# Kernel tuning notes

Hardware: AMD Instinct MI355X
Metric: run time of the kernel (lower is better)

## Reference

```python
import jax, jax.numpy as jnp
import numpy as np

RATIO = 0.8
V, F, E = 100000, 128, 3200000


def setup_inputs() -> dict:
    key = jax.random.key(0)
    k0, k1, k2, k3 = jax.random.split(key, 4)
    verts = jax.random.normal(k0, (V, F), jnp.float32)
    edges = jax.random.randint(k1, (E, 2), 0, V, dtype=jnp.int32)
    verts_idx = jnp.arange(V, dtype=jnp.int32)
    edges_idx = jnp.arange(E, dtype=jnp.int32)
    # GraphConv(in_channels=128, out=1): w0 applied to verts, w1 to summed neighbors
    w0_w = jax.random.normal(k2, (1, F), jnp.float32) * 0.05
    w0_b = jnp.zeros((1,), jnp.float32)
    w1_w = jax.random.normal(k3, (1, F), jnp.float32) * 0.05
    w1_b = jnp.zeros((1,), jnp.float32)
    return dict(verts=verts, edges=edges, verts_idx=verts_idx, edges_idx=edges_idx,
                w0_w=w0_w, w0_b=w0_b, w1_w=w1_w, w1_b=w1_b)


def graph_conv(verts, edges, w0_w, w0_b, w1_w, w1_b):
    # pytorch3d-style GraphConv: w0(v_i) + sum_{j in N(i)} w1(v_j), symmetric edges
    nv = verts.shape[0]
    vw0 = verts @ w0_w.T + w0_b            # [V,1]
    vw1 = verts @ w1_w.T + w1_b            # [V,1]
    row, col = edges[:, 0], edges[:, 1]
    nbr = jax.ops.segment_sum(vw1[col], row, num_segments=nv)
    nbr = nbr + jax.ops.segment_sum(vw1[row], col, num_segments=nv)
    return vw0 + nbr                       # [V,1]


def reference(verts, edges, verts_idx, edges_idx, w0_w, w0_b, w1_w, w1_b):
    nv = verts.shape[0]
    attn = graph_conv(verts, edges, w0_w, w0_b, w1_w, w1_b)[:, 0]  # [V]
    k = int(nv * RATIO)
    _, mask_idx = jax.lax.top_k(attn, k)
    mask_idx = jnp.sort(mask_idx)                                   # [K]
    # scatter new compacted ids into a -1 mask
    mask = jnp.full((nv,), -1, dtype=jnp.int32).at[mask_idx].set(
        jnp.arange(k, dtype=jnp.int32))
    row = mask[edges[:, 0]]
    col = mask[edges[:, 1]]
    valid = (row >= 0) & (col >= 0)
    # jit-safe compaction: stable-sort valid edges to the front, pad rest with -1
    order = jnp.argsort(~valid, stable=True)
    new_edges = jnp.stack([row, col], axis=1)[order]                # [E,2]
    valid_s = valid[order]
    new_edges = jnp.where(valid_s[:, None], new_edges, -1)
    n_edges = valid.sum()
    verts_up = verts[mask_idx] * jnp.tanh(attn[mask_idx])[:, None]  # [K,F]
    verts_idx_up = verts_idx[:k]
    edges_idx_up = jnp.where(valid_s, edges_idx[order], -1)
    return verts_up, new_edges, verts_idx_up, edges_idx_up, n_edges
```

## Files before the change

### kernel.cpp

```cpp
#include <hip/hip_runtime.h>
#include <math.h>

#define TPB 256
#define SCAN_ITEMS 4
#define SCAN_BLOCK (TPB * SCAN_ITEMS)
#define TIECAP 2048
#define HIST_BLOCKS 104
#define BW 512
#define BUCKET_BLOCKS 256
#define BIG 1024

static __device__ __forceinline__ int block_scan_excl(int v, int* lds, int& total)
{
    int lane = threadIdx.x & 63;
    int wid  = threadIdx.x >> 6;
    int x = v;
#pragma unroll
    for (int off = 1; off < 64; off <<= 1) {
        int y = __shfl_up(x, off, 64);
        if (lane >= off) x += y;
    }
    if (lane == 63) lds[wid] = x;
    __syncthreads();
    int t0 = lds[0], t1 = lds[1], t2 = lds[2], t3 = lds[3];
    int wOff = (wid > 0 ? t0 : 0) + (wid > 1 ? t1 : 0) + (wid > 2 ? t2 : 0);
    total = t0 + t1 + t2 + t3;
    __syncthreads();
    return wOff + x - v;
}

__global__ void k_init(unsigned* hist, unsigned* state, int k,
                       unsigned* cursor, int NB, int CAP)
{
    int i = threadIdx.x;
    for (int j = i; j < 1024; j += blockDim.x) hist[j] = 0u;
    if (cursor) {
        for (int j = i; j < NB; j += blockDim.x)
            cursor[j * 16] = (unsigned)(j * CAP);
    }
    if (i == 0) {
        state[0] = 0u;
        state[1] = (unsigned)k;
        state[2] = 0u;
        state[3] = 0u;
        state[4] = 0u;
    }
}

__global__ void k_dots(const float* __restrict__ verts,
                       const float* __restrict__ w0, const float* __restrict__ b0,
                       const float* __restrict__ w1, const float* __restrict__ b1,
                       long long* __restrict__ iacc, long long* __restrict__ s1q, int V)
{
    int gid  = blockIdx.x * blockDim.x + threadIdx.x;
    int v    = gid >> 6;
    int lane = gid & 63;
    if (v >= V) return;
    const float2 a  = ((const float2*)(verts + (size_t)v * 128))[lane];
    const float2 wa = ((const float2*)w0)[lane];
    const float2 wb = ((const float2*)w1)[lane];
    float p0 = a.x * wa.x + a.y * wa.y;
    float p1 = a.x * wb.x + a.y * wb.y;
#pragma unroll
    for (int off = 32; off > 0; off >>= 1) {
        p0 += __shfl_down(p0, off, 64);
        p1 += __shfl_down(p1, off, 64);
    }
    if (lane == 0) {
        double s0 = (double)p0 + (double)b0[0];
        double s1 = (double)p1 + (double)b1[0];
        iacc[v] = (long long)llrint(s0 * 1099511627776.0);
        s1q[v]  = (long long)llrint(s1 * 1099511627776.0);
    }
}

__global__ void k_scatter(const int2* __restrict__ edges, const long long* __restrict__ s1q,
                          unsigned long long* __restrict__ iacc, int E)
{
    int i = blockIdx.x * blockDim.x + threadIdx.x;
    if (i >= E) return;
    int2 e = edges[i];
    atomicAdd(&iacc[e.x], (unsigned long long)s1q[e.y]);
    atomicAdd(&iacc[e.y], (unsigned long long)s1q[e.x]);
}

__global__ void __launch_bounds__(BIG)
k_bucket(const int2* __restrict__ edges, unsigned* __restrict__ bdata,
         unsigned* __restrict__ cursor, int E, int NB, int CAP, int chunk)
{
    __shared__ unsigned cnt[256];
    __shared__ unsigned base[256];
    const int tid   = threadIdx.x;
    const int start = blockIdx.x * chunk;
    const int end   = min(E, start + chunk);
    for (int j = tid; j < 256; j += BIG) cnt[j] = 0u;
    __syncthreads();
    for (int i = start + tid; i < end; i += BIG) {
        int2 e = edges[i];
        atomicAdd(&cnt[e.x >> 9], 1u);
        atomicAdd(&cnt[e.y >> 9], 1u);
    }
    __syncthreads();
    if (tid < NB) {
        unsigned c = cnt[tid];
        base[tid] = c ? atomicAdd(&cursor[tid * 16], c) : 0u;
        cnt[tid] = 0u;
    }
    __syncthreads();
    for (int i = start + tid; i < end; i += BIG) {
        int2 e = edges[i];
        int b0 = e.x >> 9;
        unsigned p0 = base[b0] + atomicAdd(&cnt[b0], 1u);
        if (p0 < (unsigned)(b0 + 1) * (unsigned)CAP)
            bdata[p0] = ((unsigned)e.y << 9) | (unsigned)(e.x & 511);
        int b1 = e.y >> 9;
        unsigned p1 = base[b1] + atomicAdd(&cnt[b1], 1u);
        if (p1 < (unsigned)(b1 + 1) * (unsigned)CAP)
            bdata[p1] = ((unsigned)e.x << 9) | (unsigned)(e.y & 511);
    }
}

__global__ void __launch_bounds__(BIG)
k_bucket_sum(const unsigned* __restrict__ bdata, const unsigned* __restrict__ cursor,
             const long long* __restrict__ s1q, const long long* __restrict__ iacc,
             float* __restrict__ attnf, unsigned* __restrict__ keys,
             unsigned* __restrict__ hist, int V, int CAP)
{
    __shared__ unsigned long long acc[BW];
    __shared__ unsigned lh[256];
    const int b   = blockIdx.x;
    const int tid = threadIdx.x;
    for (int j = tid; j < BW;  j += BIG) acc[j] = 0ull;
    for (int j = tid; j < 256; j += BIG) lh[j] = 0u;
    __syncthreads();
    unsigned n = cursor[b * 16] - (unsigned)(b * CAP);
    if (n > (unsigned)CAP) n = (unsigned)CAP;
    const unsigned* src = bdata + (size_t)b * CAP;
    for (unsigned i = tid; i < n; i += BIG) {
        unsigned p = src[i];
        atomicAdd(&acc[p & 511u], (unsigned long long)s1q[p >> 9]);
    }
    __syncthreads();
    for (int j = tid; j < BW; j += BIG) {
        int v = b * BW + j;
        if (v < V) {
            long long tot = iacc[v] + (long long)acc[j];
            float a = (float)((double)tot * 9.094947017729282379150390625e-13);
            attnf[v] = a;
            unsigned u = __float_as_uint(a);
            unsigned key = (u & 0x80000000u) ? ~u : (u | 0x80000000u);
            keys[v] = key;
            atomicAdd(&lh[key >> 24], 1u);
        }
    }
    __syncthreads();
    for (int j = tid; j < 256; j += BIG) {
        unsigned c = lh[j];
        if (c) atomicAdd(&hist[j], c);
    }
}

__global__ void k_finalize(const long long* __restrict__ iacc, float* __restrict__ attnf,
                           unsigned* __restrict__ keys, int V)
{
    int i = blockIdx.x * blockDim.x + threadIdx.x;
    if (i >= V) return;
    float a = (float)((double)iacc[i] * 9.094947017729282379150390625e-13);
    attnf[i] = a;
    unsigned u = __float_as_uint(a);
    keys[i] = (u & 0x80000000u) ? ~u : (u | 0x80000000u);
}

__global__ void k_hist(const unsigned* __restrict__ keys, int V,
                       const unsigned* __restrict__ state, int shift,
                       unsigned* __restrict__ hist)
{
    __shared__ unsigned lh[256];
    lh[threadIdx.x] = 0u;
    __syncthreads();
    unsigned pref = 0u;
    if (shift != 24) pref = state[0] >> (shift + 8);
    int stride = gridDim.x * blockDim.x;
    for (int i = blockIdx.x * blockDim.x + threadIdx.x; i < V; i += stride) {
        unsigned key = keys[i];
        bool ok = (shift == 24) || ((key >> (shift + 8)) == pref);
        if (ok) atomicAdd(&lh[(key >> shift) & 255u], 1u);
    }
    __syncthreads();
    unsigned c = lh[threadIdx.x];
    if (c) atomicAdd(&hist[threadIdx.x], c);
}

__global__ void k_select(const unsigned* __restrict__ hist, int shift, unsigned* __restrict__ state)
{
    if (threadIdx.x != 0 || blockIdx.x != 0) return;
    unsigned kk = state[1];
    unsigned cum = 0;
    int j = 255;
    for (; j > 0; --j) {
        unsigned c = hist[j];
        if (cum + c >= kk) break;
        cum += c;
    }
    state[0] |= ((unsigned)j) << shift;
    state[1] = kk - cum;
    if (shift == 0) state[2] = state[0];
}

__global__ void k_mark(const unsigned* __restrict__ keys, int V,
                       unsigned* __restrict__ state, int* __restrict__ selFlag,
                       int* __restrict__ tieList, unsigned* __restrict__ bsums)
{
    __shared__ int lds[4];
    const unsigned T = state[2];
    int base = blockIdx.x * SCAN_BLOCK + threadIdx.x * SCAN_ITEMS;
    int f[4] = {0, 0, 0, 0};
    unsigned kv[4];
    bool full = (base + 3 < V);
    if (full) {
        uint4 q = *(const uint4*)(keys + base);
        kv[0] = q.x; kv[1] = q.y; kv[2] = q.z; kv[3] = q.w;
    } else {
#pragma unroll
        for (int t = 0; t < 4; ++t)
            kv[t] = (base + t < V) ? keys[base + t] : 0u;
    }
#pragma unroll
    for (int t = 0; t < 4; ++t) {
        if (base + t < V) {
            f[t] = kv[t] > T ? 1 : 0;
            if (kv[t] == T) {
                unsigned p = atomicAdd(&state[3], 1u);
                if (p < TIECAP) tieList[p] = base + t;
            }
        }
    }
    if (full) {
        *(int4*)(selFlag + base) = make_int4(f[0], f[1], f[2], f[3]);
    } else {
#pragma unroll
        for (int t = 0; t < 4; ++t)
            if (base + t < V) selFlag[base + t] = f[t];
    }
    int tot;
    block_scan_excl(f[0] + f[1] + f[2] + f[3], lds, tot);
    if (threadIdx.x == 0) bsums[blockIdx.x] = (unsigned)tot;
}

__global__ void k_tie_resolve(const unsigned* __restrict__ state,
                              const int* __restrict__ tieList, int* __restrict__ selFlag,
                              unsigned* __restrict__ bsums)
{
    __shared__ int s[TIECAP];
    int n  = (int)state[3];
    if (n > TIECAP) n = TIECAP;
    int kk = (int)state[1];
    int tid = threadIdx.x;
    if (kk >= n) {
        for (int i = tid; i < n; i += blockDim.x) {
            int v = tieList[i];
            selFlag[v] = 1;
            atomicAdd(&bsums[v / SCAN_BLOCK], 1u);
        }
        return;
    }
    for (int i = tid; i < n; i += blockDim.x) s[i] = tieList[i];
    __syncthreads();
    for (int i = tid; i < n; i += blockDim.x) {
        int v = s[i];
        int r = 0;
        for (int j = 0; j < n; ++j) r += (s[j] < v);
        if (r < kk) {
            selFlag[v] = 1;
            atomicAdd(&bsums[v / SCAN_BLOCK], 1u);
        }
    }
}

__global__ void k_scanB(unsigned* __restrict__ sums, int nb,
                        unsigned* __restrict__ totalOut, float* __restrict__ outF)
{
    __shared__ int lds[4];
    int tid = threadIdx.x;
    int running = 0;
    for (int base = 0; base < nb; base += TPB) {
        int i = base + tid;
        int v = (i < nb) ? (int)sums[i] : 0;
        int tot;
        int ex = block_scan_excl(v, lds, tot);
        if (i < nb) sums[i] = (unsigned)(ex + running);
        running += tot;
    }
    if (tid == 0) {
        if (totalOut) *totalOut = (unsigned)running;
        if (outF)     *outF    = (float)running;
    }
}

__global__ void k_scanC_V(const int* __restrict__ selFlag, int V,
                          const unsigned* __restrict__ bsums,
                          int* __restrict__ mask, int* __restrict__ selIdx,
                          const int* __restrict__ vidx_in, float* __restrict__ O2)
{
    __shared__ int lds[4];
    int base = blockIdx.x * SCAN_BLOCK + threadIdx.x * SCAN_ITEMS;
    int f[4] = {0, 0, 0, 0};
    if (base + 3 < V) {
        int4 q = *(const int4*)(selFlag + base);
        f[0] = q.x; f[1] = q.y; f[2] = q.z; f[3] = q.w;
    } else {
#pragma unroll
        for (int t = 0; t < 4; ++t)
            if (base + t < V) f[t] = selFlag[base + t];
    }
    int tot;
    int run = block_scan_excl(f[0] + f[1] + f[2] + f[3], lds, tot) + (int)bsums[blockIdx.x];
#pragma unroll
    for (int t = 0; t < 4; ++t) {
        int idx = base + t;
        if (idx < V) {
            if (f[t]) {
                mask[idx]    = run;
                selIdx[run]  = idx;
                O2[run]      = (float)vidx_in[run];
                run++;
            } else {
                mask[idx] = -1;
            }
        }
    }
}

__global__ void k_scanA_E(const int* __restrict__ edges, int E, const int* __restrict__ mask,
                          unsigned* __restrict__ bsums)
{
    __shared__ int lds[4];
    int base = blockIdx.x * SCAN_BLOCK + threadIdx.x * SCAN_ITEMS;
    int s = 0;
    if (base + 3 < E) {
        const int4* e4 = (const int4*)edges;
        int4 q0 = e4[(base >> 1)];
        int4 q1 = e4[(base >> 1) + 1];
        s += (mask[q0.x] >= 0 && mask[q0.y] >= 0);
        s += (mask[q0.z] >= 0 && mask[q0.w] >= 0);
        s += (mask[q1.x] >= 0 && mask[q1.y] >= 0);
        s += (mask[q1.z] >= 0 && mask[q1.w] >= 0);
    } else {
        for (int t = 0; t < 4; ++t) {
            int i = base + t;
            if (i < E) {
                int a = edges[2 * i], b = edges[2 * i + 1];
                s += (mask[a] >= 0 && mask[b] >= 0);
            }
        }
    }
    int tot;
    block_scan_excl(s, lds, tot);
    if (threadIdx.x == 0) bsums[blockIdx.x] = (unsigned)tot;
}

__global__ void k_scanC_E(const int* __restrict__ edges, int E, const int* __restrict__ mask,
                          const unsigned* __restrict__ bsums, const unsigned* __restrict__ state,
                          const int* __restrict__ eidx_in,
                          float* __restrict__ O1, float* __restrict__ O3)
{
    __shared__ int lds[4];
    __shared__ float2 lv[SCAN_BLOCK];
    __shared__ float  le[SCAN_BLOCK];
    const int start = blockIdx.x * SCAN_BLOCK;
    const int base  = start + threadIdx.x * SCAN_ITEMS;
    int fl[4] = {0, 0, 0, 0};
    float2 mv[4];
    float  ev[4];
    int s = 0;
#pragma unroll
    for (int t = 0; t < 4; ++t) {
        int i = base + t;
        if (i < E) {
            int2 e = ((const int2*)edges)[i];
            int m0 = mask[e.x], m1 = mask[e.y];
            fl[t] = (m0 >= 0 && m1 >= 0);
            if (fl[t]) {
                mv[t] = make_float2((float)m0, (float)m1);
                ev[t] = (float)eidx_in[i];
            }
            s += fl[t];
        }
    }
    int tot;
    int lrun = block_scan_excl(s, lds, tot);
#pragma unroll
    for (int t = 0; t < 4; ++t) {
        int i = base + t;
        if (i < E && fl[t]) {
            lv[lrun] = mv[t];
            le[lrun] = ev[t];
            lrun++;
        }
    }
    __syncthreads();
    const int items = min(E - start, SCAN_BLOCK);
    const unsigned vstart = bsums[blockIdx.x];
    const unsigned istart = state[4] + (unsigned)start - vstart;
    for (int j = threadIdx.x; j < tot; j += TPB) {
        ((float2*)O1)[vstart + j] = lv[j];
        O3[vstart + j] = le[j];
    }
    const int ninv = items - tot;
    for (int j = threadIdx.x; j < ninv; j += TPB) {
        ((float2*)O1)[istart + j] = make_float2(-1.0f, -1.0f);
        O3[istart + j] = -1.0f;
    }
}

__global__ void k_verts_up(const float* __restrict__ verts, const int* __restrict__ selIdx,
                           const float* __restrict__ attnf, float* __restrict__ O0, int k)
{
    int idx = blockIdx.x * blockDim.x + threadIdx.x;
    if (idx >= k * 32) return;
    int r = idx >> 5;
    int c = idx & 31;
    int v = selIdx[r];
    float t = tanhf(attnf[v]);
    float4 x = ((const float4*)verts)[(size_t)v * 32 + c];
    x.x *= t; x.y *= t; x.z *= t; x.w *= t;
    ((float4*)O0)[(size_t)r * 32 + c] = x;
}

extern "C" void kernel_launch(void* const* d_in, const int* in_sizes, int n_in,
                              void* d_out, int out_size, void* d_ws, size_t ws_size,
                              hipStream_t stream)
{
    const float* verts = (const float*)d_in[0];
    const int*   edges = (const int*)d_in[1];
    const int*   vidx  = (const int*)d_in[2];
    const int*   eidx  = (const int*)d_in[3];
    const float* w0w   = (const float*)d_in[4];
    const float* w0b   = (const float*)d_in[5];
    const float* w1w   = (const float*)d_in[6];
    const float* w1b   = (const float*)d_in[7];

    const int V = in_sizes[2];
    const int E = in_sizes[3];
    const int F = in_sizes[0] / V;
    const int k = (int)((double)V * 0.8);

    char* p = (char*)d_ws;
    auto alloc = [&](size_t bytes) -> char* {
        char* r = p;
        p += (bytes + 255) & ~(size_t)255;
        return r;
    };
    long long* iacc   = (long long*)alloc((size_t)V * 8);
    long long* s1q    = (long long*)alloc((size_t)V * 8);
    float*     attnf  = (float*)alloc((size_t)V * 4);
    unsigned*  keys   = (unsigned*)alloc((size_t)V * 4);
    int*       selFlag= (int*)alloc((size_t)V * 4);
    int*       mask   = (int*)alloc((size_t)V * 4);
    int*       selIdx = (int*)alloc((size_t)k * 4);
    int*       tieList= (int*)alloc((size_t)TIECAP * 4);
    unsigned*  hist   = (unsigned*)alloc(1024 * 4);
    unsigned*  state  = (unsigned*)alloc(64);
    const int nbV = (V + SCAN_BLOCK - 1) / SCAN_BLOCK;
    const int nbE = (E + SCAN_BLOCK - 1) / SCAN_BLOCK;
    unsigned*  bsumsV = (unsigned*)alloc((size_t)nbV * 4);
    unsigned*  bsumsE = (unsigned*)alloc((size_t)nbE * 4);

    const int NB  = (V + BW - 1) / BW;
    long long avgc = (2LL * E * BW) / (V > 0 ? V : 1);
    const int CAP = (int)(avgc + avgc / 8 + 1024);
    unsigned*  cursor = (unsigned*)alloc(256 * 64);
    unsigned*  bdata  = (unsigned*)alloc((size_t)NB * CAP * 4);
    const bool useBucket = (NB <= 256) && (V < (1 << 17)) &&
                           ((size_t)(p - (char*)d_ws) <= ws_size);

    float* out = (float*)d_out;
    float* O0 = out;
    float* O1 = O0 + (size_t)k * F;
    float* O2 = O1 + (size_t)E * 2;
    float* O3 = O2 + (size_t)k;
    float* O4 = O3 + (size_t)E;

    k_init<<<1, TPB, 0, stream>>>(hist, state, k,
                                  useBucket ? cursor : nullptr, NB, CAP);

    k_dots<<<(int)(((size_t)V * 64 + TPB - 1) / TPB), TPB, 0, stream>>>(
        verts, w0w, w0b, w1w, w1b, iacc, s1q, V);

    if (useBucket) {
        const int chunk = (E + BUCKET_BLOCKS - 1) / BUCKET_BLOCKS;
        k_bucket<<<BUCKET_BLOCKS, BIG, 0, stream>>>(
            (const int2*)edges, bdata, cursor, E, NB, CAP, chunk);
        k_bucket_sum<<<NB, BIG, 0, stream>>>(
            bdata, cursor, s1q, iacc, attnf, keys, hist, V, CAP);
    } else {
        k_scatter<<<(E + TPB - 1) / TPB, TPB, 0, stream>>>(
            (const int2*)edges, s1q, (unsigned long long*)iacc, E);
        k_finalize<<<(V + TPB - 1) / TPB, TPB, 0, stream>>>(iacc, attnf, keys, V);
    }

    for (int r = 0; r < 4; ++r) {
        int shift = 24 - 8 * r;
        if (r > 0 || !useBucket)
            k_hist<<<HIST_BLOCKS, TPB, 0, stream>>>(keys, V, state, shift, hist + 256 * r);
        k_select<<<1, 64, 0, stream>>>(hist + 256 * r, shift, state);
    }

    k_mark<<<nbV, TPB, 0, stream>>>(keys, V, state, selFlag, tieList, bsumsV);
    k_tie_resolve<<<1, TPB, 0, stream>>>(state, tieList, selFlag, bsumsV);

    k_scanB<<<1, TPB, 0, stream>>>(bsumsV, nbV, nullptr, nullptr);
    k_scanC_V<<<nbV, TPB, 0, stream>>>(selFlag, V, bsumsV, mask, selIdx, vidx, O2);

    k_scanA_E<<<nbE, TPB, 0, stream>>>(edges, E, mask, bsumsE);
    k_scanB<<<1, TPB, 0, stream>>>(bsumsE, nbE, &state[4], O4);
    k_scanC_E<<<nbE, TPB, 0, stream>>>(edges, E, mask, bsumsE, state, eidx, O1, O3);

    k_verts_up<<<(k * 32 + TPB - 1) / TPB, TPB, 0, stream>>>(verts, selIdx, attnf, O0, k);
}
```

Baseline: 379.3 us.

## Use decoupled look-back edge compaction and fuse radix-select and scan launches

Replaces the three-pass edge compaction (count, scan, scatter) with a single-pass decoupled look-back scan, in which each tile publishes its aggregate and inclusive prefix through flagged descriptors. The invalid-edge padding moves to a separate tail kernel. Radix-select passes 2-4 are merged into one 1024-thread block kernel, and the tie resolve is fused with the vertex block-sum scan. The aim is to cut kernel launches and a full re-read of edges plus mask gathers. The cost is a serial single-block radix tail over all keys and look-back spin waits that depend on tiles being scheduled in order.

```diff
diff --git a/kernel.cpp b/kernel.cpp
--- a/kernel.cpp
+++ b/kernel.cpp
@@ -10,6 +10,10 @@
 #define BUCKET_BLOCKS 256
 #define BIG 1024
 
+#define FLAG_AGG  (1ull << 62)
+#define FLAG_PRE  (2ull << 62)
+#define FLAG_MASK (3ull << 62)
+
 static __device__ __forceinline__ int block_scan_excl(int v, int* lds, int& total)
 {
     int lane = threadIdx.x & 63;
@@ -30,14 +34,16 @@
 }
 
 __global__ void k_init(unsigned* hist, unsigned* state, int k,
-                       unsigned* cursor, int NB, int CAP)
+                       unsigned* cursor, int NB, int CAP,
+                       unsigned long long* desc, int nTiles)
 {
     int i = threadIdx.x;
-    for (int j = i; j < 1024; j += blockDim.x) hist[j] = 0u;
+    for (int j = i; j < 256; j += blockDim.x) hist[j] = 0u;
     if (cursor) {
         for (int j = i; j < NB; j += blockDim.x)
             cursor[j * 16] = (unsigned)(j * CAP);
     }
+    for (int j = i; j < nTiles; j += blockDim.x) desc[j] = 0ull;
     if (i == 0) {
         state[0] = 0u;
         state[1] = (unsigned)k;
@@ -171,40 +177,58 @@
     keys[i] = (u & 0x80000000u) ? ~u : (u | 0x80000000u);
 }
 
-__global__ void k_hist(const unsigned* __restrict__ keys, int V,
-                       const unsigned* __restrict__ state, int shift,
-                       unsigned* __restrict__ hist)
+__global__ void k_hist(const unsigned* __restrict__ keys, int V, unsigned* __restrict__ hist)
 {
     __shared__ unsigned lh[256];
     lh[threadIdx.x] = 0u;
     __syncthreads();
-    unsigned pref = 0u;
-    if (shift != 24) pref = state[0] >> (shift + 8);
     int stride = gridDim.x * blockDim.x;
-    for (int i = blockIdx.x * blockDim.x + threadIdx.x; i < V; i += stride) {
-        unsigned key = keys[i];
-        bool ok = (shift == 24) || ((key >> (shift + 8)) == pref);
-        if (ok) atomicAdd(&lh[(key >> shift) & 255u], 1u);
-    }
+    for (int i = blockIdx.x * blockDim.x + threadIdx.x; i < V; i += stride)
+        atomicAdd(&lh[keys[i] >> 24], 1u);
     __syncthreads();
     unsigned c = lh[threadIdx.x];
     if (c) atomicAdd(&hist[threadIdx.x], c);
 }
 
-__global__ void k_select(const unsigned* __restrict__ hist, int shift, unsigned* __restrict__ state)
-{
-    if (threadIdx.x != 0 || blockIdx.x != 0) return;
-    unsigned kk = state[1];
-    unsigned cum = 0;
-    int j = 255;
-    for (; j > 0; --j) {
-        unsigned c = hist[j];
-        if (cum + c >= kk) break;
-        cum += c;
-    }
-    state[0] |= ((unsigned)j) << shift;
-    state[1] = kk - cum;
-    if (shift == 0) state[2] = state[0];
+__global__ void __launch_bounds__(BIG)
+k_radix_tail(const unsigned* __restrict__ keys, int V,
+             const unsigned* __restrict__ hist0, unsigned* __restrict__ state)
+{
+    __shared__ unsigned lh[256];
+    __shared__ unsigned spref, skk;
+    const int tid = threadIdx.x;
+    if (tid == 0) {
+        unsigned kk = state[1];
+        unsigned cum = 0; int j = 255;
+        for (; j > 0; --j) { unsigned c = hist0[j]; if (cum + c >= kk) break; cum += c; }
+        spref = ((unsigned)j) << 24;
+        skk = kk - cum;
+    }
+    __syncthreads();
+    for (int shift = 16; shift >= 0; shift -= 8) {
+        for (int j = tid; j < 256; j += BIG) lh[j] = 0u;
+        __syncthreads();
+        const unsigned prefHi = spref >> (shift + 8);
+        for (int i = tid; i < V; i += BIG) {
+            unsigned key = keys[i];
+            if ((key >> (shift + 8)) == prefHi)
+                atomicAdd(&lh[(key >> shift) & 255u], 1u);
+        }
+        __syncthreads();
+        if (tid == 0) {
+            unsigned kk = skk;
+            unsigned cum = 0; int j = 255;
+            for (; j > 0; --j) { unsigned c = lh[j]; if (cum + c >= kk) break; cum += c; }
+            spref |= ((unsigned)j) << shift;
+            skk = kk - cum;
+        }
+        __syncthreads();
+    }
+    if (tid == 0) {
+        state[0] = spref;
+        state[1] = skk;
+        state[2] = spref;
+    }
 }
 
 __global__ void k_mark(const unsigned* __restrict__ keys, int V,
@@ -247,11 +271,12 @@
     if (threadIdx.x == 0) bsums[blockIdx.x] = (unsigned)tot;
 }
 
-__global__ void k_tie_resolve(const unsigned* __restrict__ state,
-                              const int* __restrict__ tieList, int* __restrict__ selFlag,
-                              unsigned* __restrict__ bsums)
+__global__ void k_vfinish(const unsigned* __restrict__ state,
+                          const int* __restrict__ tieList, int* __restrict__ selFlag,
+                          unsigned* __restrict__ bsums, int nb)
 {
     __shared__ int s[TIECAP];
+    __shared__ int lds[4];
     int n  = (int)state[3];
     if (n > TIECAP) n = TIECAP;
     int kk = (int)state[1];
@@ -262,38 +287,28 @@
             selFlag[v] = 1;
             atomicAdd(&bsums[v / SCAN_BLOCK], 1u);
         }
-        return;
-    }
-    for (int i = tid; i < n; i += blockDim.x) s[i] = tieList[i];
-    __syncthreads();
-    for (int i = tid; i < n; i += blockDim.x) {
-        int v = s[i];
-        int r = 0;
-        for (int j = 0; j < n; ++j) r += (s[j] < v);
-        if (r < kk) {
-            selFlag[v] = 1;
-            atomicAdd(&bsums[v / SCAN_BLOCK], 1u);
-        }
-    }
-}
-
-__global__ void k_scanB(unsigned* __restrict__ sums, int nb,
-                        unsigned* __restrict__ totalOut, float* __restrict__ outF)
-{
-    __shared__ int lds[4];
-    int tid = threadIdx.x;
+    } else {
+        for (int i = tid; i < n; i += blockDim.x) s[i] = tieList[i];
+        __syncthreads();
+        for (int i = tid; i < n; i += blockDim.x) {
+            int v = s[i];
+            int r = 0;
+            for (int j = 0; j < n; ++j) r += (s[j] < v);
+            if (r < kk) {
+                selFlag[v] = 1;
+                atomicAdd(&bsums[v / SCAN_BLOCK], 1u);
+            }
+        }
+    }
+    __syncthreads();
     int running = 0;
     for (int base = 0; base < nb; base += TPB) {
         int i = base + tid;
-        int v = (i < nb) ? (int)sums[i] : 0;
+        int v = (i < nb) ? (int)bsums[i] : 0;
         int tot;
         int ex = block_scan_excl(v, lds, tot);
-        if (i < nb) sums[i] = (unsigned)(ex + running);
+        if (i < nb) bsums[i] = (unsigned)(ex + running);
         running += tot;
-    }
-    if (tid == 0) {
-        if (totalOut) *totalOut = (unsigned)running;
-        if (outF)     *outF    = (float)running;
     }
 }
 
@@ -331,43 +346,19 @@
     }
 }
 
-__global__ void k_scanA_E(const int* __restrict__ edges, int E, const int* __restrict__ mask,
-                          unsigned* __restrict__ bsums)
-{
-    __shared__ int lds[4];
-    int base = blockIdx.x * SCAN_BLOCK + threadIdx.x * SCAN_ITEMS;
-    int s = 0;
-    if (base + 3 < E) {
-        const int4* e4 = (const int4*)edges;
-        int4 q0 = e4[(base >> 1)];
-        int4 q1 = e4[(base >> 1) + 1];
-        s += (mask[q0.x] >= 0 && mask[q0.y] >= 0);
-        s += (mask[q0.z] >= 0 && mask[q0.w] >= 0);
-        s += (mask[q1.x] >= 0 && mask[q1.y] >= 0);
-        s += (mask[q1.z] >= 0 && mask[q1.w] >= 0);
-    } else {
-        for (int t = 0; t < 4; ++t) {
-            int i = base + t;
-            if (i < E) {
-                int a = edges[2 * i], b = edges[2 * i + 1];
-                s += (mask[a] >= 0 && mask[b] >= 0);
-            }
-        }
-    }
-    int tot;
-    block_scan_excl(s, lds, tot);
-    if (threadIdx.x == 0) bsums[blockIdx.x] = (unsigned)tot;
-}
-
-__global__ void k_scanC_E(const int* __restrict__ edges, int E, const int* __restrict__ mask,
-                          const unsigned* __restrict__ bsums, const unsigned* __restrict__ state,
-                          const int* __restrict__ eidx_in,
-                          float* __restrict__ O1, float* __restrict__ O3)
+__global__ void k_part_E(const int* __restrict__ edges, int E, const int* __restrict__ mask,
+                         const int* __restrict__ eidx_in,
+                         unsigned long long* __restrict__ desc,
+                         unsigned* __restrict__ state,
+                         float* __restrict__ O1, float* __restrict__ O3,
+                         float* __restrict__ O4)
 {
     __shared__ int lds[4];
     __shared__ float2 lv[SCAN_BLOCK];
     __shared__ float  le[SCAN_BLOCK];
-    const int start = blockIdx.x * SCAN_BLOCK;
+    __shared__ unsigned sbase;
+    const int tile  = blockIdx.x;
+    const int start = tile * SCAN_BLOCK;
     const int base  = start + threadIdx.x * SCAN_ITEMS;
     int fl[4] = {0, 0, 0, 0};
     float2 mv[4];
@@ -398,19 +389,68 @@
             lrun++;
         }
     }
-    __syncthreads();
-    const int items = min(E - start, SCAN_BLOCK);
-    const unsigned vstart = bsums[blockIdx.x];
-    const unsigned istart = state[4] + (unsigned)start - vstart;
+    if (threadIdx.x == 0) {
+        unsigned long long v = (tile == 0 ? FLAG_PRE : FLAG_AGG) | (unsigned long long)(unsigned)tot;
+        __hip_atomic_store(&desc[tile], v, __ATOMIC_RELEASE, __HIP_MEMORY_SCOPE_AGENT);
+    }
+    if (threadIdx.x < 64) {
+        unsigned run = 0;
+        if (tile > 0) {
+            int j = tile - 1;
+            while (true) {
+                int idx = j - (int)threadIdx.x;
+                unsigned long long d = 0ull;
+                if (idx >= 0)
+                    d = __hip_atomic_load(&desc[idx], __ATOMIC_ACQUIRE, __HIP_MEMORY_SCOPE_AGENT);
+                unsigned long long fbits = d & FLAG_MASK;
+                bool isPre = (idx >= 0) && (fbits == FLAG_PRE);
+                bool isInv = (idx >= 0) && (fbits == 0ull);
+                unsigned long long bPre = __ballot(isPre);
+                unsigned long long bInv = __ballot(isInv);
+                int firstPre = bPre ? (__ffsll((long long)bPre) - 1) : 64;
+                int firstInv = bInv ? (__ffsll((long long)bInv) - 1) : 64;
+                if (firstInv < firstPre) continue;
+                unsigned contrib = 0;
+                if (idx >= 0 && (int)threadIdx.x <= firstPre)
+                    contrib = (unsigned)(d & ~FLAG_MASK);
+#pragma unroll
+                for (int off = 32; off > 0; off >>= 1)
+                    contrib += __shfl_down(contrib, off, 64);
+                contrib = __shfl(contrib, 0, 64);
+                run += contrib;
+                if (firstPre < 64) break;
+                j -= 64;
+            }
+        }
+        if (threadIdx.x == 0) {
+            sbase = run;
+            __hip_atomic_store(&desc[tile],
+                               FLAG_PRE | (unsigned long long)(unsigned)(run + tot),
+                               __ATOMIC_RELEASE, __HIP_MEMORY_SCOPE_AGENT);
+            if (tile == (int)gridDim.x - 1) {
+                state[4] = run + (unsigned)tot;
+                *O4 = (float)(run + (unsigned)tot);
+            }
+        }
+    }
+    __syncthreads();
+    const unsigned vstart = sbase;
     for (int j = threadIdx.x; j < tot; j += TPB) {
         ((float2*)O1)[vstart + j] = lv[j];
         O3[vstart + j] = le[j];
     }
-    const int ninv = items - tot;
-    for (int j = threadIdx.x; j < ninv; j += TPB) {
-        ((float2*)O1)[istart + j] = make_float2(-1.0f, -1.0f);
-        O3[istart + j] = -1.0f;
-    }
+}
+
+__global__ void k_tail_E(const unsigned* __restrict__ state, int E,
+                         float* __restrict__ O1, float* __restrict__ O3)
+{
+    __shared__ unsigned nv;
+    if (threadIdx.x == 0) nv = state[4];
+    __syncthreads();
+    int i = blockIdx.x * blockDim.x + threadIdx.x;
+    if (i >= E || i < (int)nv) return;
+    ((float2*)O1)[i] = make_float2(-1.0f, -1.0f);
+    O3[i] = -1.0f;
 }
 
 __global__ void k_verts_up(const float* __restrict__ verts, const int* __restrict__ selIdx,
@@ -459,12 +499,12 @@
     int*       mask   = (int*)alloc((size_t)V * 4);
     int*       selIdx = (int*)alloc((size_t)k * 4);
     int*       tieList= (int*)alloc((size_t)TIECAP * 4);
-    unsigned*  hist   = (unsigned*)alloc(1024 * 4);
+    unsigned*  hist   = (unsigned*)alloc(256 * 4);
     unsigned*  state  = (unsigned*)alloc(64);
     const int nbV = (V + SCAN_BLOCK - 1) / SCAN_BLOCK;
     const int nbE = (E + SCAN_BLOCK - 1) / SCAN_BLOCK;
     unsigned*  bsumsV = (unsigned*)alloc((size_t)nbV * 4);
-    unsigned*  bsumsE = (unsigned*)alloc((size_t)nbE * 4);
+    unsigned long long* desc = (unsigned long long*)alloc((size_t)nbE * 8);
 
     const int NB  = (V + BW - 1) / BW;
     long long avgc = (2LL * E * BW) / (V > 0 ? V : 1);
@@ -482,7 +522,7 @@
     float* O4 = O3 + (size_t)E;
 
     k_init<<<1, TPB, 0, stream>>>(hist, state, k,
-                                  useBucket ? cursor : nullptr, NB, CAP);
+                                  useBucket ? cursor : nullptr, NB, CAP, desc, nbE);
 
     k_dots<<<(int)(((size_t)V * 64 + TPB - 1) / TPB), TPB, 0, stream>>>(
         verts, w0w, w0b, w1w, w1b, iacc, s1q, V);
@@ -497,24 +537,17 @@
         k_scatter<<<(E + TPB - 1) / TPB, TPB, 0, stream>>>(
             (const int2*)edges, s1q, (unsigned long long*)iacc, E);
         k_finalize<<<(V + TPB - 1) / TPB, TPB, 0, stream>>>(iacc, attnf, keys, V);
-    }
-
-    for (int r = 0; r < 4; ++r) {
-        int shift = 24 - 8 * r;
-        if (r > 0 || !useBucket)
-            k_hist<<<HIST_BLOCKS, TPB, 0, stream>>>(keys, V, state, shift, hist + 256 * r);
-        k_select<<<1, 64, 0, stream>>>(hist + 256 * r, shift, state);
-    }
+        k_hist<<<HIST_BLOCKS, TPB, 0, stream>>>(keys, V, hist);
+    }
+
+    k_radix_tail<<<1, BIG, 0, stream>>>(keys, V, hist, state);
 
     k_mark<<<nbV, TPB, 0, stream>>>(keys, V, state, selFlag, tieList, bsumsV);
-    k_tie_resolve<<<1, TPB, 0, stream>>>(state, tieList, selFlag, bsumsV);
-
-    k_scanB<<<1, TPB, 0, stream>>>(bsumsV, nbV, nullptr, nullptr);
+    k_vfinish<<<1, TPB, 0, stream>>>(state, tieList, selFlag, bsumsV, nbV);
     k_scanC_V<<<nbV, TPB, 0, stream>>>(selFlag, V, bsumsV, mask, selIdx, vidx, O2);
 
-    k_scanA_E<<<nbE, TPB, 0, stream>>>(edges, E, mask, bsumsE);
-    k_scanB<<<1, TPB, 0, stream>>>(bsumsE, nbE, &state[4], O4);
-    k_scanC_E<<<nbE, TPB, 0, stream>>>(edges, E, mask, bsumsE, state, eidx, O1, O3);
+    k_part_E<<<nbE, TPB, 0, stream>>>(edges, E, mask, eidx, desc, state, O1, O3, O4);
+    k_tail_E<<<(E + BIG - 1) / BIG, BIG, 0, stream>>>(state, E, O1, O3);
 
     k_verts_up<<<(k * 32 + TPB - 1) / TPB, TPB, 0, stream>>>(verts, selIdx, attnf, O0, k);
 }
```

Result: slower. 674.1 us (+77.8%).

## Fuse radix-select passes into one block and merge tie-resolve with scan

Applied to the files above, without the earlier changes.

Replaces the three later histogram+select kernel pairs of the radix top-k threshold search with one single-block kernel. That kernel resolves the first digit from the global histogram, then loops over the remaining digits with shared-memory histograms. It also folds tie resolution and the vertex block-sum scan into one kernel. The goal is to cut kernel launches and inter-kernel dependency gaps, at the cost of a single 1024-thread block scanning all V keys three times serially.

```diff
diff --git a/kernel.cpp b/kernel.cpp
--- a/kernel.cpp
+++ b/kernel.cpp
@@ -33,7 +33,7 @@
                        unsigned* cursor, int NB, int CAP)
 {
     int i = threadIdx.x;
-    for (int j = i; j < 1024; j += blockDim.x) hist[j] = 0u;
+    for (int j = i; j < 256; j += blockDim.x) hist[j] = 0u;
     if (cursor) {
         for (int j = i; j < NB; j += blockDim.x)
             cursor[j * 16] = (unsigned)(j * CAP);
@@ -171,40 +171,58 @@
     keys[i] = (u & 0x80000000u) ? ~u : (u | 0x80000000u);
 }
 
-__global__ void k_hist(const unsigned* __restrict__ keys, int V,
-                       const unsigned* __restrict__ state, int shift,
-                       unsigned* __restrict__ hist)
+__global__ void k_hist(const unsigned* __restrict__ keys, int V, unsigned* __restrict__ hist)
 {
     __shared__ unsigned lh[256];
     lh[threadIdx.x] = 0u;
     __syncthreads();
-    unsigned pref = 0u;
-    if (shift != 24) pref = state[0] >> (shift + 8);
     int stride = gridDim.x * blockDim.x;
-    for (int i = blockIdx.x * blockDim.x + threadIdx.x; i < V; i += stride) {
-        unsigned key = keys[i];
-        bool ok = (shift == 24) || ((key >> (shift + 8)) == pref);
-        if (ok) atomicAdd(&lh[(key >> shift) & 255u], 1u);
-    }
+    for (int i = blockIdx.x * blockDim.x + threadIdx.x; i < V; i += stride)
+        atomicAdd(&lh[keys[i] >> 24], 1u);
     __syncthreads();
     unsigned c = lh[threadIdx.x];
     if (c) atomicAdd(&hist[threadIdx.x], c);
 }
 
-__global__ void k_select(const unsigned* __restrict__ hist, int shift, unsigned* __restrict__ state)
-{
-    if (threadIdx.x != 0 || blockIdx.x != 0) return;
-    unsigned kk = state[1];
-    unsigned cum = 0;
-    int j = 255;
-    for (; j > 0; --j) {
-        unsigned c = hist[j];
-        if (cum + c >= kk) break;
-        cum += c;
-    }
-    state[0] |= ((unsigned)j) << shift;
-    state[1] = kk - cum;
-    if (shift == 0) state[2] = state[0];
+__global__ void __launch_bounds__(BIG)
+k_radix_tail(const unsigned* __restrict__ keys, int V,
+             const unsigned* __restrict__ hist0, unsigned* __restrict__ state)
+{
+    __shared__ unsigned lh[256];
+    __shared__ unsigned spref, skk;
+    const int tid = threadIdx.x;
+    if (tid == 0) {
+        unsigned kk = state[1];
+        unsigned cum = 0; int j = 255;
+        for (; j > 0; --j) { unsigned c = hist0[j]; if (cum + c >= kk) break; cum += c; }
+        spref = ((unsigned)j) << 24;
+        skk = kk - cum;
+    }
+    __syncthreads();
+    for (int shift = 16; shift >= 0; shift -= 8) {
+        for (int j = tid; j < 256; j += BIG) lh[j] = 0u;
+        __syncthreads();
+        const unsigned prefHi = spref >> (shift + 8);
+        for (int i = tid; i < V; i += BIG) {
+            unsigned key = keys[i];
+            if ((key >> (shift + 8)) == prefHi)
+                atomicAdd(&lh[(key >> shift) & 255u], 1u);
+        }
+        __syncthreads();
+        if (tid == 0) {
+            unsigned kk = skk;
+            unsigned cum = 0; int j = 255;
+            for (; j > 0; --j) { unsigned c = lh[j]; if (cum + c >= kk) break; cum += c; }
+            spref |= ((unsigned)j) << shift;
+            skk = kk - cum;
+        }
+        __syncthreads();
+    }
+    if (tid == 0) {
+        state[0] = spref;
+        state[1] = skk;
+        state[2] = spref;
+    }
 }
 
 __global__ void k_mark(const unsigned* __restrict__ keys, int V,
@@ -247,11 +265,12 @@
     if (threadIdx.x == 0) bsums[blockIdx.x] = (unsigned)tot;
 }
 
-__global__ void k_tie_resolve(const unsigned* __restrict__ state,
-                              const int* __restrict__ tieList, int* __restrict__ selFlag,
-                              unsigned* __restrict__ bsums)
+__global__ void k_vfinish(const unsigned* __restrict__ state,
+                          const int* __restrict__ tieList, int* __restrict__ selFlag,
+                          unsigned* __restrict__ bsums, int nb)
 {
     __shared__ int s[TIECAP];
+    __shared__ int lds[4];
     int n  = (int)state[3];
     if (n > TIECAP) n = TIECAP;
     int kk = (int)state[1];
@@ -262,38 +281,28 @@
             selFlag[v] = 1;
             atomicAdd(&bsums[v / SCAN_BLOCK], 1u);
         }
-        return;
-    }
-    for (int i = tid; i < n; i += blockDim.x) s[i] = tieList[i];
-    __syncthreads();
-    for (int i = tid; i < n; i += blockDim.x) {
-        int v = s[i];
-        int r = 0;
-        for (int j = 0; j < n; ++j) r += (s[j] < v);
-        if (r < kk) {
-            selFlag[v] = 1;
-            atomicAdd(&bsums[v / SCAN_BLOCK], 1u);
-        }
-    }
-}
-
-__global__ void k_scanB(unsigned* __restrict__ sums, int nb,
-                        unsigned* __restrict__ totalOut, float* __restrict__ outF)
-{
-    __shared__ int lds[4];
-    int tid = threadIdx.x;
+    } else {
+        for (int i = tid; i < n; i += blockDim.x) s[i] = tieList[i];
+        __syncthreads();
+        for (int i = tid; i < n; i += blockDim.x) {
+            int v = s[i];
+            int r = 0;
+            for (int j = 0; j < n; ++j) r += (s[j] < v);
+            if (r < kk) {
+                selFlag[v] = 1;
+                atomicAdd(&bsums[v / SCAN_BLOCK], 1u);
+            }
+        }
+    }
+    __syncthreads();
     int running = 0;
     for (int base = 0; base < nb; base += TPB) {
         int i = base + tid;
-        int v = (i < nb) ? (int)sums[i] : 0;
+        int v = (i < nb) ? (int)bsums[i] : 0;
         int tot;
         int ex = block_scan_excl(v, lds, tot);
-        if (i < nb) sums[i] = (unsigned)(ex + running);
+        if (i < nb) bsums[i] = (unsigned)(ex + running);
         running += tot;
-    }
-    if (tid == 0) {
-        if (totalOut) *totalOut = (unsigned)running;
-        if (outF)     *outF    = (float)running;
     }
 }
 
@@ -359,6 +368,26 @@
     if (threadIdx.x == 0) bsums[blockIdx.x] = (unsigned)tot;
 }
 
+__global__ void k_scanB(unsigned* __restrict__ sums, int nb,
+                        unsigned* __restrict__ totalOut, float* __restrict__ outF)
+{
+    __shared__ int lds[4];
+    int tid = threadIdx.x;
+    int running = 0;
+    for (int base = 0; base < nb; base += TPB) {
+        int i = base + tid;
+        int v = (i < nb) ? (int)sums[i] : 0;
+        int tot;
+        int ex = block_scan_excl(v, lds, tot);
+        if (i < nb) sums[i] = (unsigned)(ex + running);
+        running += tot;
+    }
+    if (tid == 0) {
+        if (totalOut) *totalOut = (unsigned)running;
+        if (outF)     *outF    = (float)running;
+    }
+}
+
 __global__ void k_scanC_E(const int* __restrict__ edges, int E, const int* __restrict__ mask,
                           const unsigned* __restrict__ bsums, const unsigned* __restrict__ state,
                           const int* __restrict__ eidx_in,
@@ -459,7 +488,7 @@
     int*       mask   = (int*)alloc((size_t)V * 4);
     int*       selIdx = (int*)alloc((size_t)k * 4);
     int*       tieList= (int*)alloc((size_t)TIECAP * 4);
-    unsigned*  hist   = (unsigned*)alloc(1024 * 4);
+    unsigned*  hist   = (unsigned*)alloc(256 * 4);
     unsigned*  state  = (unsigned*)alloc(64);
     const int nbV = (V + SCAN_BLOCK - 1) / SCAN_BLOCK;
     const int nbE = (E + SCAN_BLOCK - 1) / SCAN_BLOCK;
@@ -497,19 +526,13 @@
         k_scatter<<<(E + TPB - 1) / TPB, TPB, 0, stream>>>(
             (const int2*)edges, s1q, (unsigned long long*)iacc, E);
         k_finalize<<<(V + TPB - 1) / TPB, TPB, 0, stream>>>(iacc, attnf, keys, V);
-    }
-
-    for (int r = 0; r < 4; ++r) {
-        int shift = 24 - 8 * r;
-        if (r > 0 || !useBucket)
-            k_hist<<<HIST_BLOCKS, TPB, 0, stream>>>(keys, V, state, shift, hist + 256 * r);
-        k_select<<<1, 64, 0, stream>>>(hist + 256 * r, shift, state);
-    }
+        k_hist<<<HIST_BLOCKS, TPB, 0, stream>>>(keys, V, hist);
+    }
+
+    k_radix_tail<<<1, BIG, 0, stream>>>(keys, V, hist, state);
 
     k_mark<<<nbV, TPB, 0, stream>>>(keys, V, state, selFlag, tieList, bsumsV);
-    k_tie_resolve<<<1, TPB, 0, stream>>>(state, tieList, selFlag, bsumsV);
-
-    k_scanB<<<1, TPB, 0, stream>>>(bsumsV, nbV, nullptr, nullptr);
+    k_vfinish<<<1, TPB, 0, stream>>>(state, tieList, selFlag, bsumsV, nbV);
     k_scanC_V<<<nbV, TPB, 0, stream>>>(selFlag, V, bsumsV, mask, selIdx, vidx, O2);
 
     k_scanA_E<<<nbE, TPB, 0, stream>>>(edges, E, mask, bsumsE);
```

New measurement: 421.1 us. 11.0% more time.
